# Performance work log

Hardware: AMD Instinct MI355X
Metric: run time of the kernel (lower is better)

The kernel has to match this reference:

```python
import jax, jax.numpy as jnp
import numpy as np

K = 7          # kernel_size
PAD = K // 2
NAZ, NEL = 12, 5
HID = 64
IC = 2         # input_channels == num_instruments
OC = 2         # output_channels (stereo)
EPS = 1e-5


def conv1d_same(x, w, b):
    # x: (N, Cin, T), w: (Cout, Cin, K) -> (N, Cout, T); cross-correlation like torch
    y = jax.lax.conv_general_dilated(x, w, (1,), 'SAME',
                                     dimension_numbers=('NCH', 'OIH', 'NCH'))
    return y + b[None, :, None]


def batchnorm(x, g, bt):
    # training-mode BatchNorm1d: biased batch stats over (N, T)
    mean = x.mean(axis=(0, 2), keepdims=True)
    var = x.var(axis=(0, 2), keepdims=True)
    return (x - mean) * jax.lax.rsqrt(var + EPS) * g[None, :, None] + bt[None, :, None]


def lrelu(x):
    return jnp.where(x >= 0, x, 0.2 * x)


def setup_inputs() -> dict:
    key = jax.random.key(0)
    ks = jax.random.split(key, 16)
    d = {}
    d['x'] = jax.random.normal(ks[0], (8, IC, 131072), dtype=jnp.float32)
    # spatial_param_net
    d['W1'] = jax.random.normal(ks[1], (HID, IC, K), dtype=jnp.float32) * 0.1
    d['b1'] = jnp.zeros((HID,), jnp.float32)
    d['g1'] = jnp.ones((HID,), jnp.float32)
    d['be1'] = jnp.zeros((HID,), jnp.float32)
    d['W2'] = jax.random.normal(ks[2], (2 * HID, HID, K), dtype=jnp.float32) * 0.05
    d['b2'] = jnp.zeros((2 * HID,), jnp.float32)
    d['g2'] = jnp.ones((2 * HID,), jnp.float32)
    d['be2'] = jnp.zeros((2 * HID,), jnp.float32)
    d['W3'] = jax.random.normal(ks[3], (IC * 3, 2 * HID, K), dtype=jnp.float32) * 0.05
    d['b3'] = jnp.zeros((IC * 3,), jnp.float32)
    # HRTF table: (num_azimuth*num_elevation, output_channels, K)
    d['hrtf'] = jax.random.normal(ks[4], (NAZ * NEL, OC, K), dtype=jnp.float32)
    # binaural_renderer (first conv in-channels = input_channels = 2)
    d['RW1'] = jax.random.normal(ks[5], (HID, IC, K), dtype=jnp.float32) * 0.1
    d['rb1'] = jnp.zeros((HID,), jnp.float32)
    d['rg1'] = jnp.ones((HID,), jnp.float32)
    d['rbe1'] = jnp.zeros((HID,), jnp.float32)
    d['RW2'] = jax.random.normal(ks[6], (2 * HID, HID, K), dtype=jnp.float32) * 0.05
    d['rb2'] = jnp.zeros((2 * HID,), jnp.float32)
    d['rg2'] = jnp.ones((2 * HID,), jnp.float32)
    d['rbe2'] = jnp.zeros((2 * HID,), jnp.float32)
    d['RW3'] = jax.random.normal(ks[7], (OC, 2 * HID, K), dtype=jnp.float32) * 0.05
    d['rb3'] = jnp.zeros((OC,), jnp.float32)
    return d


def reference(x, W1, b1, g1, be1, W2, b2, g2, be2, W3, b3, hrtf,
              RW1, rb1, rg1, rbe1, RW2, rb2, rg2, rbe2, RW3, rb3):
    B, I, T = x.shape
    # spatial parameter network
    h = lrelu(batchnorm(conv1d_same(x, W1, b1), g1, be1))
    h = lrelu(batchnorm(conv1d_same(h, W2, b2), g2, be2))
    sp = jnp.tanh(conv1d_same(h, W3, b3)).reshape(B, I, 3, T)
    # only t=0 of azimuth/elevation/distance is used (matches torch loop)
    az = (sp[:, :, 0, 0] + 1.0) * 0.5 * (NAZ - 1)
    el = (sp[:, :, 1, 0] + 1.0) * 0.5 * (NEL - 1)
    dist = (sp[:, :, 2, 0] + 1.0) * 0.5 * 0.9 + 0.1      # (B, I)
    az_i = jnp.clip(az.astype(jnp.int32), 0, NAZ - 1)
    el_i = jnp.clip(el.astype(jnp.int32), 0, NEL - 1)
    idx = el_i * NAZ + az_i                               # (B, I)
    wg = hrtf[idx]                                        # (B, I, OC, K) gathered filters
    # per-(b,i) conv1d with its gathered HRTF filter, scale by distance, sum over instruments
    xp = jnp.pad(x, ((0, 0), (0, 0), (PAD, PAD)))
    windows = jnp.stack([xp[:, :, k:k + T] for k in range(K)], axis=2)  # (B, I, K, T)
    summed = jnp.einsum('bikt,bick,bi->bct', windows, wg, dist)          # (B, OC, T)
    # binaural renderer
    h = lrelu(batchnorm(conv1d_same(summed, RW1, rb1), rg1, rbe1))
    h = lrelu(batchnorm(conv1d_same(h, RW2, rb2), rg2, rbe2))
    return jnp.tanh(conv1d_same(h, RW3, rb3))
```

## Files before the change

### kernel.cpp

```cpp
#include <hip/hip_runtime.h>
#include <hip/hip_fp16.h>
#include <cstddef>


#define TLEN 131072
#define NB 8
#define NICH 2
#define NHID 64
#define NH2 128
#define EPSV 1e-5f
#define CNTF 1048576.0f
#define FT 120
#define FGRID 1093
#define XCH 2048

typedef _Float16 f16x8 __attribute__((ext_vector_type(8)));
typedef float f32x4 __attribute__((ext_vector_type(4)));

__device__ __forceinline__ float lrelu(float v) { return fmaxf(v, 0.2f * v); }
__device__ __forceinline__ unsigned short h16(float v) {
  return __half_as_ushort(__float2half(v));
}
__device__ __forceinline__ float fh16(unsigned short u) {
  return __half2float(__ushort_as_half(u));
}
__device__ __forceinline__ float ftanh(float x) {
  float e = __expf(2.f * x);
  return 1.f - 2.f / (e + 1.f);
}

__global__ __launch_bounds__(256) void prep_weights(
    const float* __restrict__ W2c, const float* __restrict__ RW2c,
    const float* __restrict__ RW3c,
    const float* __restrict__ W1c, const float* __restrict__ RW1c,
    unsigned short* __restrict__ w2sp, unsigned short* __restrict__ w2re,
    unsigned short* __restrict__ w3g,
    unsigned short* __restrict__ w1sp, unsigned short* __restrict__ w1re)
{
  int e = blockIdx.x * 256 + threadIdx.x;
  if (e < 114688) {
    int e2 = (e >= 57344) ? e - 57344 : e;
    int frag = e2 >> 9, within = e2 & 511;
    int c = frag >> 3, mt = frag & 7;
    int mn = within >> 5, kk = within & 31;
    int o = mt * 16 + mn;
    int tap = c >> 1, ch = (c & 1) * 32 + kk;
    const float* src = (e >= 57344) ? RW2c : W2c;
    unsigned short* dst = (e >= 57344) ? w2re : w2sp;
    dst[e2] = h16(src[(o * 64 + ch) * 7 + tap]);
  } else if (e < 116736) {
    int e2 = e - 114688;
    int c = e2 >> 9, within = e2 & 511;
    int m = within >> 5, kk = within & 31;
    int ch = c * 32 + kk;
    w3g[e2] = (m < 14) ? h16(RW3c[((m / 7) * 128 + ch) * 7 + (m % 7)])
                       : (unsigned short)0;
  } else if (e < 120832) {
    int e2 = e - 116736;
    int which = (e2 >= 2048);
    int e3 = e2 & 2047;
    int m = e3 >> 9, w = e3 & 511;
    int mn = w >> 5, K = w & 31;
    int i = K >> 4, kk = K & 15;
    const float* src = which ? RW1c : W1c;
    unsigned short* dst = which ? w1re : w1sp;
    dst[e3] = (kk < 7) ? h16(src[(m * 16 + mn) * 14 + i * 7 + kk])
                       : (unsigned short)0;
  }
}

__global__ __launch_bounds__(256) void xcorr_stats(
    const float* __restrict__ z, float* __restrict__ partials)
{
  const int b = blockIdx.x >> 6;
  const int t0 = (blockIdx.x & 63) * XCH;
  __shared__ float zs[2][XCH + 8];
  __shared__ float redx[4][30];
  for (int i = 0; i < 2; ++i)
    for (int j = threadIdx.x; j < XCH + 7; j += 256) {
      int tg = t0 + j;
      zs[i][j] = (tg < TLEN) ? z[(b * 2 + i) * TLEN + tg] : 0.f;
    }
  __syncthreads();

  float acc[30];
  #pragma unroll
  for (int q = 0; q < 30; ++q) acc[q] = 0.f;
  const int tb = threadIdx.x * 8;
  #pragma unroll
  for (int tt = 0; tt < 8; ++tt) {
    int j = tb + tt;
    float z0 = zs[0][j], z1 = zs[1][j];
    acc[28] += z0; acc[29] += z1;
    #pragma unroll
    for (int d = 0; d < 7; ++d) {
      float a0 = zs[0][j + d], a1 = zs[1][j + d];
      acc[d]      += z0 * a0;
      acc[7 + d]  += z0 * a1;
      acc[14 + d] += z1 * a0;
      acc[21 + d] += z1 * a1;
    }
  }
  #pragma unroll
  for (int q = 0; q < 30; ++q)
    #pragma unroll
    for (int m = 1; m <= 32; m <<= 1)
      acc[q] += __shfl_xor(acc[q], m, 64);
  const int lane = threadIdx.x & 63, wv = threadIdx.x >> 6;
  if (lane == 0)
    #pragma unroll
    for (int q = 0; q < 30; ++q) redx[wv][q] = acc[q];
  __syncthreads();
  if (threadIdx.x < 30)
    partials[blockIdx.x * 30 + threadIdx.x] =
        redx[0][threadIdx.x] + redx[1][threadIdx.x] +
        redx[2][threadIdx.x] + redx[3][threadIdx.x];
}

__global__ __launch_bounds__(256) void assemble_coef1(
    const float* __restrict__ partials, int nblocks,
    const float* __restrict__ W1c, const float* __restrict__ b1c,
    const float* __restrict__ g, const float* __restrict__ be,
    float* __restrict__ coef)
{
  __shared__ float R[30];
  __shared__ float pr[8][30];
  __shared__ float w1s[64 * 14];
  for (int e = threadIdx.x; e < 64 * 14; e += 256) w1s[e] = W1c[e];
  if (threadIdx.x < 240) {
    int q = threadIdx.x % 30, chunk = threadIdx.x / 30;
    float s = 0.f;
    for (int j = chunk; j < nblocks; j += 8) s += partials[j * 30 + q];
    pr[chunk][q] = s;
  }
  __syncthreads();
  if (threadIdx.x < 30) {
    float s = 0.f;
    #pragma unroll
    for (int c = 0; c < 8; ++c) s += pr[c][threadIdx.x];
    R[threadIdx.x] = s;
  }
  __syncthreads();
  if (threadIdx.x < 64) {
    int o = threadIdx.x;
    const float* w = &w1s[o * 14];
    float b1v = b1c[o];
    float sy = 0.f;
    #pragma unroll
    for (int i = 0; i < 2; ++i)
      #pragma unroll
      for (int k = 0; k < 7; ++k) sy += w[i * 7 + k] * R[28 + i];
    float syy = 0.f;
    #pragma unroll
    for (int i = 0; i < 2; ++i)
      #pragma unroll
      for (int k = 0; k < 7; ++k) {
        float wv = w[i * 7 + k];
        #pragma unroll
        for (int i2 = 0; i2 < 2; ++i2)
          #pragma unroll
          for (int k2 = 0; k2 < 7; ++k2) {
            int d = k2 - k;
            float r = (d >= 0) ? R[i * 14 + i2 * 7 + d]
                               : R[i2 * 14 + i * 7 - d];
            syy += wv * w[i2 * 7 + k2] * r;
          }
      }
    float S1 = CNTF * b1v + sy;
    float S2 = 2.f * b1v * S1 - CNTF * b1v * b1v + syy;
    float mean = S1 / CNTF;
    float var = S2 / CNTF - mean * mean;
    float a = g[o] * rsqrtf(var + EPSV);
    coef[o] = a;
    coef[64 + o] = be[o] - mean * a;
  }
}

__global__ __launch_bounds__(256) void reduce_coef(
    const float* __restrict__ partials, int nblocks, int C,
    const float* __restrict__ bso,
    const float* __restrict__ g, const float* __restrict__ be,
    float* __restrict__ coef)
{
  const int c = blockIdx.x;
  float s = 0.f, ss = 0.f;
  for (int j = threadIdx.x; j < nblocks; j += 256) {
    s  += partials[j * 2 * C + c];
    ss += partials[j * 2 * C + C + c];
  }
  #pragma unroll
  for (int off = 32; off >= 1; off >>= 1) {
    s  += __shfl_down(s, off, 64);
    ss += __shfl_down(ss, off, 64);
  }
  __shared__ float rs[4], rss[4];
  const int lane = threadIdx.x & 63, wv = threadIdx.x >> 6;
  if (lane == 0) { rs[wv] = s; rss[wv] = ss; }
  __syncthreads();
  if (threadIdx.x == 0) {
    float st  = rs[0] + rs[1] + rs[2] + rs[3];
    float sst = rss[0] + rss[1] + rss[2] + rss[3];
    float mean = st / CNTF;
    float var  = sst / CNTF - mean * mean;
    float a = g[c] * rsqrtf(var + EPSV);
    float d = be[c] - mean * a;
    coef[c] = a;
    coef[C + c] = d;
    coef[2 * C + c] = d + a * bso[c];
  }
}

__device__ __forceinline__ void stage_x(
    int t0, int xoff, const float* __restrict__ xin, int b, float* xs)
{
  for (int e = threadIdx.x; e < 2 * 168; e += 256) {
    int i = e / 168, j = e % 168;
    int tg = t0 - xoff + j;
    xs[e] = (tg >= 0 && tg < TLEN) ? xin[(b * NICH + i) * TLEN + tg] : 0.f;
  }
}

template<int HOF>
__device__ __forceinline__ void h1_mfma(
    int t0, const float* xs, unsigned short* xw,
    const unsigned short* __restrict__ w1f,
    const float* __restrict__ coef1, const float* __restrict__ b1c,
    unsigned short* h1f)
{
  for (int e = threadIdx.x; e < 144 * 2; e += 256) {
    int n = e >> 1, i = e & 1;
    const float* xp = &xs[i * 168 + n];
    unsigned short hv[7];
    #pragma unroll
    for (int kk = 0; kk < 7; ++kk) hv[kk] = h16(xp[kk]);
    *(uint4*)(xw + n * 32 + i * 16) = make_uint4(
        hv[0] | ((unsigned)hv[1] << 16), hv[2] | ((unsigned)hv[3] << 16),
        hv[4] | ((unsigned)hv[5] << 16), (unsigned)hv[6]);
    *(uint4*)(xw + n * 32 + i * 16 + 8) = make_uint4(0, 0, 0, 0);
  }
  __syncthreads();

  const int lane = threadIdx.x & 63;
  const int wv = threadIdx.x >> 6;
  const int mn = lane & 15, quad = lane >> 4;
  f16x8 A1 = *(const f16x8*)(w1f + wv * 512 + mn * 32 + quad * 8);
  f32x4 acc1[9];
  #pragma unroll
  for (int nt = 0; nt < 9; ++nt) {
    f32x4 z = {0.f, 0.f, 0.f, 0.f};
    acc1[nt] = z;
  }
  #pragma unroll
  for (int nt = 0; nt < 9; ++nt) {
    f16x8 bb = *(const f16x8*)(xw + (nt * 16 + mn) * 32 + quad * 8);
    acc1[nt] = __builtin_amdgcn_mfma_f32_16x16x32_f16(A1, bb, acc1[nt], 0, 0, 0);
  }
  const int ch0 = wv * 16 + quad * 4;
  float a1v[4], dd[4];
  #pragma unroll
  for (int r = 0; r < 4; ++r) {
    a1v[r] = coef1[ch0 + r];
    dd[r]  = coef1[64 + ch0 + r] + a1v[r] * b1c[ch0 + r];
  }
  #pragma unroll
  for (int nt = 0; nt < 9; ++nt) {
    int n = nt * 16 + mn;
    int t = t0 - HOF + n;
    bool ok = (t >= 0) && (t < TLEN);
    unsigned us[4];
    #pragma unroll
    for (int r = 0; r < 4; ++r) {
      float v = lrelu(a1v[r] * acc1[nt][r] + dd[r]);
      us[r] = h16(ok ? v : 0.f);
    }
    *(uint2*)(h1f + n * 72 + ch0) =
        make_uint2(us[0] | (us[1] << 16), us[2] | (us[3] << 16));
  }
}

__global__ __launch_bounds__(256, 4) void conv2_stats_mfma(
    const float* __restrict__ xin,
    const unsigned short* __restrict__ w1f, const float* __restrict__ b1c,
    const float* __restrict__ coef1,
    const unsigned short* __restrict__ w2f,
    const float* __restrict__ b2c,
    float* __restrict__ partials)
{
  const int b  = blockIdx.x >> 10;
  const int t0 = (blockIdx.x & 1023) * 128;

  __shared__ __align__(16) char smem[31296];
  unsigned short* h1f = (unsigned short*)smem;
  float* xs = (float*)(smem + 20736);
  unsigned short* xw = (unsigned short*)(smem + 22080);
  float* redS = (float*)smem;
  float* redSS= (float*)(smem + 8704);

  stage_x(t0, 6, xin, b, xs);
  __syncthreads();
  h1_mfma<3>(t0, xs, xw, w1f, coef1, b1c, h1f);
  __syncthreads();

  const int lane = threadIdx.x & 63;
  const int wv = threadIdx.x >> 6;
  const int mn = lane & 15, quad = lane >> 4;

  f32x4 acc[2][8];
  #pragma unroll
  for (int mt = 0; mt < 2; ++mt)
    #pragma unroll
    for (int nt = 0; nt < 8; ++nt) {
      f32x4 z = {0.f, 0.f, 0.f, 0.f};
      acc[mt][nt] = z;
    }

  f16x8 ca[2], na[2];
  auto loadA = [&](int c, f16x8 (&A)[2]) {
    #pragma unroll
    for (int mt = 0; mt < 2; ++mt)
      A[mt] = *(const f16x8*)(w2f + (c * 8 + wv * 2 + mt) * 512 + mn * 32 + quad * 8);
  };
  loadA(0, ca);
  #pragma unroll
  for (int c = 0; c < 14; ++c) {
    if (c < 13) loadA(c + 1, na);
    const int tap = c >> 1;
    const int ch0 = (c & 1) * 32 + quad * 8;
    #pragma unroll
    for (int nt = 0; nt < 8; ++nt) {
      f16x8 bb = *(const f16x8*)(h1f + (nt * 16 + mn + tap) * 72 + ch0);
      acc[0][nt] = __builtin_amdgcn_mfma_f32_16x16x32_f16(ca[0], bb, acc[0][nt], 0, 0, 0);
      acc[1][nt] = __builtin_amdgcn_mfma_f32_16x16x32_f16(ca[1], bb, acc[1][nt], 0, 0, 0);
    }
    ca[0] = na[0]; ca[1] = na[1];
  }
  __syncthreads();

  #pragma unroll
  for (int mt = 0; mt < 2; ++mt)
    #pragma unroll
    for (int r = 0; r < 4; ++r) {
      int o = (wv * 2 + mt) * 16 + quad * 4 + r;
      float bo = b2c[o];
      float s = 0.f, ss = 0.f;
      #pragma unroll
      for (int nt = 0; nt < 8; ++nt) {
        float v = acc[mt][nt][r] + bo;
        s += v; ss += v * v;
      }
      redS[o * 17 + mn] = s;
      redSS[o * 17 + mn] = ss;
    }
  __syncthreads();
  {
    int o = threadIdx.x & 127;
    const float* src = (threadIdx.x < 128) ? redS : redSS;
    float s = 0.f;
    #pragma unroll
    for (int j = 0; j < 16; ++j) s += src[o * 17 + j];
    partials[blockIdx.x * 256 + threadIdx.x] = s;
  }
}

__global__ __launch_bounds__(256) void finalize_spatial(
    const float* __restrict__ x,
    const float* __restrict__ W1c, const float* __restrict__ b1c,
    const float* __restrict__ coef1,
    const float* __restrict__ W2c, const float* __restrict__ b2c,
    const float* __restrict__ coef2,
    const float* __restrict__ W3c, const float* __restrict__ b3c,
    const float* __restrict__ hrtf, float* __restrict__ wgbuf)
{
  __shared__ float xl[NB * 2 * 16];
  __shared__ float h1l[NB * 64 * 10];
  __shared__ float h2l[NB * NH2 * 4];
  __shared__ float sp[48];
  const int tid = threadIdx.x;
  {
    int bb = tid >> 5, i = (tid >> 4) & 1, j = tid & 15;
    int t = j - 6;
    xl[tid] = (t >= 0) ? x[(bb * 2 + i) * TLEN + t] : 0.f;
  }
  __syncthreads();
  for (int e = tid; e < NB * 64; e += 256) {
    int bb = e >> 6, ch = e & 63;
    float a1 = coef1[ch], d1 = coef1[64 + ch], bo = b1c[ch];
    for (int tt = 0; tt < 10; ++tt) {
      float acc = bo;
      #pragma unroll
      for (int i2 = 0; i2 < 2; ++i2)
        #pragma unroll
        for (int k = 0; k < 7; ++k)
          acc += xl[(bb * 2 + i2) * 16 + tt + k] * W1c[ch * 14 + i2 * 7 + k];
      float v = lrelu(a1 * acc + d1);
      h1l[(bb * 64 + ch) * 10 + tt] = (tt >= 3) ? v : 0.f;
    }
  }
  __syncthreads();
  for (int e = tid; e < NB * NH2; e += 256) {
    int bb = e >> 7, o = e & 127;
    float a2 = coef2[o], d2 = coef2[NH2 + o], bo = b2c[o];
    float acc[4] = {bo, bo, bo, bo};
    for (int i = 0; i < 64; ++i)
      #pragma unroll
      for (int k = 0; k < 7; ++k) {
        float w = W2c[(o * 64 + i) * 7 + k];
        #pragma unroll
        for (int t = 0; t < 4; ++t)
          acc[t] += h1l[(bb * 64 + i) * 10 + t + k] * w;
      }
    #pragma unroll
    for (int t = 0; t < 4; ++t)
      h2l[(bb * NH2 + o) * 4 + t] = lrelu(a2 * acc[t] + d2);
  }
  __syncthreads();
  if (tid < 48) {
    int bb = tid / 6, c3 = tid % 6;
    float acc = b3c[c3];
    for (int c = 0; c < NH2; ++c)
      #pragma unroll
      for (int k = 3; k < 7; ++k)
        acc += h2l[(bb * NH2 + c) * 4 + (k - 3)] * W3c[(c3 * NH2 + c) * 7 + k];
    sp[tid] = tanhf(acc);
  }
  __syncthreads();
  if (tid < 16) {
    int bb = tid >> 1, i = tid & 1;
    float az = (sp[bb * 6 + i * 3 + 0] + 1.f) * 0.5f * 11.f;
    float el = (sp[bb * 6 + i * 3 + 1] + 1.f) * 0.5f * 4.f;
    float dist = (sp[bb * 6 + i * 3 + 2] + 1.f) * 0.5f * 0.9f + 0.1f;
    int azi = min(max((int)az, 0), 11);
    int eli = min(max((int)el, 0), 4);
    int idx = eli * 12 + azi;
    for (int e = 0; e < 14; ++e)
      wgbuf[(bb * 2 + i) * 14 + e] = hrtf[idx * 14 + e] * dist;
  }
}

__global__ __launch_bounds__(256) void mix_kernel(
    const float* __restrict__ x, const float* __restrict__ wgbuf,
    float* __restrict__ summed)
{
  const int b = blockIdx.x >> 7;
  const int t0 = (blockIdx.x & 127) * 1024 + threadIdx.x * 4;
  float wv[2][2][7];
  #pragma unroll
  for (int i = 0; i < 2; ++i)
    #pragma unroll
    for (int c = 0; c < 2; ++c)
      #pragma unroll
      for (int k = 0; k < 7; ++k)
        wv[i][c][k] = wgbuf[(b * 2 + i) * 14 + c * 7 + k];
  float acc[2][4] = {{0.f, 0.f, 0.f, 0.f}, {0.f, 0.f, 0.f, 0.f}};
  #pragma unroll
  for (int i = 0; i < 2; ++i) {
    float xl[12];
    #pragma unroll
    for (int j = 0; j < 12; ++j) {
      int tg = t0 - 4 + j;
      xl[j] = (tg >= 0 && tg < TLEN) ? x[(b * 2 + i) * TLEN + tg] : 0.f;
    }
    #pragma unroll
    for (int c = 0; c < 2; ++c)
      #pragma unroll
      for (int k = 0; k < 7; ++k)
        #pragma unroll
        for (int tt = 0; tt < 4; ++tt)
          acc[c][tt] += xl[tt + k + 1] * wv[i][c][k];
  }
  #pragma unroll
  for (int c = 0; c < 2; ++c)
    *reinterpret_cast<float4*>(&summed[(b * 2 + c) * TLEN + t0]) =
        make_float4(acc[c][0], acc[c][1], acc[c][2], acc[c][3]);
}

__global__ __launch_bounds__(256, 4) void conv2_final_mfma(
    const float* __restrict__ xin,
    const unsigned short* __restrict__ w1f, const float* __restrict__ b1c,
    const float* __restrict__ coef1,
    const unsigned short* __restrict__ w2f,
    const float* __restrict__ coef2,
    const unsigned short* __restrict__ w3g, const float* __restrict__ rb3c,
    float* __restrict__ out)
{
  const int b  = blockIdx.y;
  const int t0 = blockIdx.x * FT;

  __shared__ __align__(16) char smem[39936];
  unsigned short* h1f = (unsigned short*)smem;
  float* xs = (float*)(smem + 20736);
  unsigned short* xw = (unsigned short*)(smem + 22080);
  unsigned short* h2t = (unsigned short*)smem;
  unsigned short* dq  = (unsigned short*)(smem + 34816);

  stage_x(t0, 9, xin, b, xs);
  __syncthreads();
  h1_mfma<6>(t0, xs, xw, w1f, coef1, b1c, h1f);
  __syncthreads();

  const int lane = threadIdx.x & 63;
  const int wv = threadIdx.x >> 6;
  const int mn = lane & 15, quad = lane >> 4;

  f32x4 acc[2][8];
  #pragma unroll
  for (int mt = 0; mt < 2; ++mt)
    #pragma unroll
    for (int nt = 0; nt < 8; ++nt) {
      f32x4 z = {0.f, 0.f, 0.f, 0.f};
      acc[mt][nt] = z;
    }

  f16x8 ca[2], na[2];
  auto loadA = [&](int c, f16x8 (&A)[2]) {
    #pragma unroll
    for (int mt = 0; mt < 2; ++mt)
      A[mt] = *(const f16x8*)(w2f + (c * 8 + wv * 2 + mt) * 512 + mn * 32 + quad * 8);
  };
  loadA(0, ca);
  #pragma unroll
  for (int c = 0; c < 14; ++c) {
    if (c < 13) loadA(c + 1, na);
    const int tap = c >> 1;
    const int ch0 = (c & 1) * 32 + quad * 8;
    #pragma unroll
    for (int nt = 0; nt < 8; ++nt) {
      f16x8 bb = *(const f16x8*)(h1f + (nt * 16 + mn + tap) * 72 + ch0);
      acc[0][nt] = __builtin_amdgcn_mfma_f32_16x16x32_f16(ca[0], bb, acc[0][nt], 0, 0, 0);
      acc[1][nt] = __builtin_amdgcn_mfma_f32_16x16x32_f16(ca[1], bb, acc[1][nt], 0, 0, 0);
    }
    ca[0] = na[0]; ca[1] = na[1];
  }

  float a2v[2][4], dd2[2][4];
  #pragma unroll
  for (int mt = 0; mt < 2; ++mt)
    #pragma unroll
    for (int r = 0; r < 4; ++r) {
      int o = (wv * 2 + mt) * 16 + quad * 4 + r;
      a2v[mt][r] = coef2[o];
      dd2[mt][r] = coef2[2 * NH2 + o];
    }
  __syncthreads();

  #pragma unroll
  for (int nt = 0; nt < 8; ++nt) {
    int jp = nt * 16 + mn;
    int t = t0 - 3 + jp;
    bool ok = (t >= 0) && (t < TLEN);
    #pragma unroll
    for (int mt = 0; mt < 2; ++mt) {
      int obase = (wv * 2 + mt) * 16 + quad * 4;
      unsigned us[4];
      #pragma unroll
      for (int r = 0; r < 4; ++r) {
        float v = lrelu(a2v[mt][r] * acc[mt][nt][r] + dd2[mt][r]);
        us[r] = h16(ok ? v : 0.f);
      }
      *(uint2*)(h2t + jp * 136 + obase) =
          make_uint2(us[0] | (us[1] << 16), us[2] | (us[3] << 16));
    }
  }
  __syncthreads();

  const int nt0 = wv * 2;
  f32x4 acc3[2];
  #pragma unroll
  for (int i = 0; i < 2; ++i) {
    f32x4 z = {0.f, 0.f, 0.f, 0.f};
    acc3[i] = z;
  }
  #pragma unroll
  for (int c = 0; c < 4; ++c) {
    f16x8 A3 = *(const f16x8*)(w3g + c * 512 + mn * 32 + quad * 8);
    #pragma unroll
    for (int i = 0; i < 2; ++i) {
      f16x8 bb = *(const f16x8*)(h2t + ((nt0 + i) * 16 + mn) * 136 + c * 32 + quad * 8);
      acc3[i] = __builtin_amdgcn_mfma_f32_16x16x32_f16(A3, bb, acc3[i], 0, 0, 0);
    }
  }
  #pragma unroll
  for (int i = 0; i < 2; ++i) {
    int n = (nt0 + i) * 16 + mn;
    unsigned us[4];
    #pragma unroll
    for (int r = 0; r < 4; ++r) us[r] = h16(acc3[i][r]);
    *(uint2*)(dq + n * 20 + quad * 4) =
        make_uint2(us[0] | (us[1] << 16), us[2] | (us[3] << 16));
  }
  __syncthreads();

  {
    int tid = threadIdx.x;
    if (tid < 240) {
      int oc = (tid >= FT) ? 1 : 0;
      int u = tid - oc * FT;
      float s = rb3c[oc];
      #pragma unroll
      for (int tap = 0; tap < 7; ++tap)
        s += fh16(dq[(u + tap) * 20 + oc * 7 + tap]);
      int t = t0 + u;
      if (t < TLEN) out[(b * 2 + oc) * TLEN + t] = ftanh(s);
    }
  }
}

extern "C" void kernel_launch(void* const* d_in, const int* in_sizes, int n_in,
                              void* d_out, int out_size, void* d_ws, size_t ws_size,
                              hipStream_t stream)
{
  (void)in_sizes; (void)n_in; (void)out_size; (void)ws_size;
  const float* x    = (const float*)d_in[0];
  const float* W1   = (const float*)d_in[1];
  const float* b1   = (const float*)d_in[2];
  const float* g1   = (const float*)d_in[3];
  const float* be1  = (const float*)d_in[4];
  const float* W2   = (const float*)d_in[5];
  const float* b2   = (const float*)d_in[6];
  const float* g2   = (const float*)d_in[7];
  const float* be2  = (const float*)d_in[8];
  const float* W3   = (const float*)d_in[9];
  const float* b3   = (const float*)d_in[10];
  const float* hrtf = (const float*)d_in[11];
  const float* RW1  = (const float*)d_in[12];
  const float* rb1  = (const float*)d_in[13];
  const float* rg1  = (const float*)d_in[14];
  const float* rbe1 = (const float*)d_in[15];
  const float* RW2  = (const float*)d_in[16];
  const float* rb2  = (const float*)d_in[17];
  const float* rg2  = (const float*)d_in[18];
  const float* rbe2 = (const float*)d_in[19];
  const float* RW3  = (const float*)d_in[20];
  const float* rb3  = (const float*)d_in[21];
  float* out = (float*)d_out;

  float* partialsB = (float*)d_out;

  char* ws = (char*)d_ws;
  float* partialsA      = (float*)(ws + 0);
  float* summed         = (float*)(ws + 524288);
  float* coef1          = (float*)(ws + 8912896);
  float* coef2          = (float*)(ws + 8913408);
  float* coefR1         = (float*)(ws + 8914944);
  float* coefR2         = (float*)(ws + 8915456);
  float* wgbuf          = (float*)(ws + 8916992);
  unsigned short* w2sp  = (unsigned short*)(ws + 8918016);
  unsigned short* w2re  = (unsigned short*)(ws + 9032704);
  unsigned short* w3g   = (unsigned short*)(ws + 9147392);
  unsigned short* w1sp  = (unsigned short*)(ws + 9151488);
  unsigned short* w1re  = (unsigned short*)(ws + 9155584);

  prep_weights<<<472, 256, 0, stream>>>(W2, RW2, RW3, W1, RW1,
                                        w2sp, w2re, w3g, w1sp, w1re);
  xcorr_stats<<<512, 256, 0, stream>>>(x, partialsA);
  assemble_coef1<<<1, 256, 0, stream>>>(partialsA, 512, W1, b1, g1, be1, coef1);
  conv2_stats_mfma<<<8192, 256, 0, stream>>>(x, w1sp, b1, coef1, w2sp, b2,
                                             partialsB);
  reduce_coef<<<128, 256, 0, stream>>>(partialsB, 8192, 128, b2, g2, be2, coef2);
  finalize_spatial<<<1, 256, 0, stream>>>(x, W1, b1, coef1, W2, b2, coef2,
                                          W3, b3, hrtf, wgbuf);
  mix_kernel<<<1024, 256, 0, stream>>>(x, wgbuf, summed);
  xcorr_stats<<<512, 256, 0, stream>>>(summed, partialsA);
  assemble_coef1<<<1, 256, 0, stream>>>(partialsA, 512, RW1, rb1, rg1, rbe1, coefR1);
  conv2_stats_mfma<<<8192, 256, 0, stream>>>(summed, w1re, rb1, coefR1,
                                             w2re, rb2, partialsB);
  reduce_coef<<<128, 256, 0, stream>>>(partialsB, 8192, 128, rb2, rg2, rbe2, coefR2);
  conv2_final_mfma<<<dim3(FGRID, NB), 256, 0, stream>>>(
      summed, w1re, rb1, coefR1, w2re, coefR2, w3g, rb3, out);
}
```

Baseline: 648.9 us.

## Store renderer conv2 activations in fp16 and skip recomputation in final pass

The renderer's stats pass now also writes the pre-norm conv2 output (fp16, 128 channels per sample) to a large workspace buffer. The final pass then only applies the BN affine and leaky ReLU, runs conv3 and writes the output, instead of recomputing conv1 and conv2. This swaps a large MFMA recompute for about 256MB of extra global write and read traffic. It falls back to the old path when the workspace is too small.

```diff
diff --git a/kernel.cpp b/kernel.cpp
--- a/kernel.cpp
+++ b/kernel.cpp
@@ -278,21 +278,24 @@
   }
 }
 
+template<bool SAVE>
 __global__ __launch_bounds__(256, 4) void conv2_stats_mfma(
     const float* __restrict__ xin,
     const unsigned short* __restrict__ w1f, const float* __restrict__ b1c,
     const float* __restrict__ coef1,
     const unsigned short* __restrict__ w2f,
     const float* __restrict__ b2c,
-    float* __restrict__ partials)
+    float* __restrict__ partials,
+    unsigned short* __restrict__ h2out)
 {
   const int b  = blockIdx.x >> 10;
   const int t0 = (blockIdx.x & 1023) * 128;
 
-  __shared__ __align__(16) char smem[31296];
+  __shared__ __align__(16) char smem[34816];
   unsigned short* h1f = (unsigned short*)smem;
   float* xs = (float*)(smem + 20736);
   unsigned short* xw = (unsigned short*)(smem + 22080);
+  unsigned short* h2t = (unsigned short*)smem;
   float* redS = (float*)smem;
   float* redSS= (float*)(smem + 8704);
 
@@ -335,6 +338,29 @@
     ca[0] = na[0]; ca[1] = na[1];
   }
   __syncthreads();
+
+  if (SAVE) {
+    #pragma unroll
+    for (int nt = 0; nt < 8; ++nt) {
+      int jp = nt * 16 + mn;
+      #pragma unroll
+      for (int mt = 0; mt < 2; ++mt) {
+        int obase = (wv * 2 + mt) * 16 + quad * 4;
+        unsigned us[4];
+        #pragma unroll
+        for (int r = 0; r < 4; ++r) us[r] = h16(acc[mt][nt][r]);
+        *(uint2*)(h2t + jp * 136 + obase) =
+            make_uint2(us[0] | (us[1] << 16), us[2] | (us[3] << 16));
+      }
+    }
+    __syncthreads();
+    for (int e = threadIdx.x; e < 2048; e += 256) {
+      int row = e >> 4, c8 = (e & 15) * 8;
+      *(uint4*)(h2out + (size_t)(b * TLEN + t0 + row) * 128 + c8) =
+          *(const uint4*)(h2t + row * 136 + c8);
+    }
+    __syncthreads();
+  }
 
   #pragma unroll
   for (int mt = 0; mt < 2; ++mt)
@@ -605,11 +631,99 @@
   }
 }
 
+__global__ __launch_bounds__(256, 4) void render_final_light(
+    const unsigned short* __restrict__ h2s,
+    const float* __restrict__ coef2,
+    const unsigned short* __restrict__ w3g, const float* __restrict__ rb3c,
+    float* __restrict__ out)
+{
+  const int b  = blockIdx.y;
+  const int t0 = blockIdx.x * FT;
+
+  __shared__ __align__(16) char smem[39936];
+  unsigned short* h2t = (unsigned short*)smem;
+  unsigned short* dq  = (unsigned short*)(smem + 34816);
+
+  const int c8 = (threadIdx.x & 15) * 8;
+  float a2r[8], d2r[8];
+  #pragma unroll
+  for (int j = 0; j < 8; ++j) {
+    a2r[j] = coef2[c8 + j];
+    d2r[j] = coef2[2 * NH2 + c8 + j];
+  }
+  for (int e = threadIdx.x; e < 2048; e += 256) {
+    int row = e >> 4;
+    int t = t0 - 3 + row;
+    uint4 pk = make_uint4(0, 0, 0, 0);
+    if (t >= 0 && t < TLEN) {
+      uint4 rv = *(const uint4*)(h2s + ((size_t)(b * TLEN + t) * 128 + c8));
+      unsigned w[4] = {rv.x, rv.y, rv.z, rv.w};
+      unsigned ow[4];
+      #pragma unroll
+      for (int j = 0; j < 4; ++j) {
+        float vlo = lrelu(a2r[2 * j] * fh16((unsigned short)(w[j] & 0xffff)) +
+                          d2r[2 * j]);
+        float vhi = lrelu(a2r[2 * j + 1] * fh16((unsigned short)(w[j] >> 16)) +
+                          d2r[2 * j + 1]);
+        ow[j] = (unsigned)h16(vlo) | ((unsigned)h16(vhi) << 16);
+      }
+      pk = make_uint4(ow[0], ow[1], ow[2], ow[3]);
+    }
+    *(uint4*)(h2t + row * 136 + c8) = pk;
+  }
+  __syncthreads();
+
+  const int lane = threadIdx.x & 63;
+  const int wv = threadIdx.x >> 6;
+  const int mn = lane & 15, quad = lane >> 4;
+
+  const int nt0 = wv * 2;
+  f32x4 acc3[2];
+  #pragma unroll
+  for (int i = 0; i < 2; ++i) {
+    f32x4 z = {0.f, 0.f, 0.f, 0.f};
+    acc3[i] = z;
+  }
+  #pragma unroll
+  for (int c = 0; c < 4; ++c) {
+    f16x8 A3 = *(const f16x8*)(w3g + c * 512 + mn * 32 + quad * 8);
+    #pragma unroll
+    for (int i = 0; i < 2; ++i) {
+      f16x8 bb = *(const f16x8*)(h2t + ((nt0 + i) * 16 + mn) * 136 + c * 32 + quad * 8);
+      acc3[i] = __builtin_amdgcn_mfma_f32_16x16x32_f16(A3, bb, acc3[i], 0, 0, 0);
+    }
+  }
+  #pragma unroll
+  for (int i = 0; i < 2; ++i) {
+    int n = (nt0 + i) * 16 + mn;
+    unsigned us[4];
+    #pragma unroll
+    for (int r = 0; r < 4; ++r) us[r] = h16(acc3[i][r]);
+    *(uint2*)(dq + n * 20 + quad * 4) =
+        make_uint2(us[0] | (us[1] << 16), us[2] | (us[3] << 16));
+  }
+  __syncthreads();
+
+  {
+    int tid = threadIdx.x;
+    if (tid < 240) {
+      int oc = (tid >= FT) ? 1 : 0;
+      int u = tid - oc * FT;
+      float s = rb3c[oc];
+      #pragma unroll
+      for (int tap = 0; tap < 7; ++tap)
+        s += fh16(dq[(u + tap) * 20 + oc * 7 + tap]);
+      int t = t0 + u;
+      if (t < TLEN) out[(b * 2 + oc) * TLEN + t] = ftanh(s);
+    }
+  }
+}
+
 extern "C" void kernel_launch(void* const* d_in, const int* in_sizes, int n_in,
                               void* d_out, int out_size, void* d_ws, size_t ws_size,
                               hipStream_t stream)
 {
-  (void)in_sizes; (void)n_in; (void)out_size; (void)ws_size;
+  (void)in_sizes; (void)n_in; (void)out_size;
   const float* x    = (const float*)d_in[0];
   const float* W1   = (const float*)d_in[1];
   const float* b1   = (const float*)d_in[2];
@@ -649,22 +763,35 @@
   unsigned short* w3g   = (unsigned short*)(ws + 9147392);
   unsigned short* w1sp  = (unsigned short*)(ws + 9151488);
   unsigned short* w1re  = (unsigned short*)(ws + 9155584);
+  unsigned short* h2s   = (unsigned short*)(ws + 16777216);
+  const size_t WS_NEEDED_BIG = 16777216ull + 268435456ull;
+  const bool big = ws_size >= WS_NEEDED_BIG;
 
   prep_weights<<<472, 256, 0, stream>>>(W2, RW2, RW3, W1, RW1,
                                         w2sp, w2re, w3g, w1sp, w1re);
   xcorr_stats<<<512, 256, 0, stream>>>(x, partialsA);
   assemble_coef1<<<1, 256, 0, stream>>>(partialsA, 512, W1, b1, g1, be1, coef1);
-  conv2_stats_mfma<<<8192, 256, 0, stream>>>(x, w1sp, b1, coef1, w2sp, b2,
-                                             partialsB);
+  conv2_stats_mfma<false><<<8192, 256, 0, stream>>>(x, w1sp, b1, coef1, w2sp,
+                                                    b2, partialsB, nullptr);
   reduce_coef<<<128, 256, 0, stream>>>(partialsB, 8192, 128, b2, g2, be2, coef2);
   finalize_spatial<<<1, 256, 0, stream>>>(x, W1, b1, coef1, W2, b2, coef2,
                                           W3, b3, hrtf, wgbuf);
   mix_kernel<<<1024, 256, 0, stream>>>(x, wgbuf, summed);
   xcorr_stats<<<512, 256, 0, stream>>>(summed, partialsA);
   assemble_coef1<<<1, 256, 0, stream>>>(partialsA, 512, RW1, rb1, rg1, rbe1, coefR1);
-  conv2_stats_mfma<<<8192, 256, 0, stream>>>(summed, w1re, rb1, coefR1,
-                                             w2re, rb2, partialsB);
+  if (big) {
+    conv2_stats_mfma<true><<<8192, 256, 0, stream>>>(summed, w1re, rb1, coefR1,
+                                                     w2re, rb2, partialsB, h2s);
+  } else {
+    conv2_stats_mfma<false><<<8192, 256, 0, stream>>>(summed, w1re, rb1, coefR1,
+                                                      w2re, rb2, partialsB, nullptr);
+  }
   reduce_coef<<<128, 256, 0, stream>>>(partialsB, 8192, 128, rb2, rg2, rbe2, coefR2);
-  conv2_final_mfma<<<dim3(FGRID, NB), 256, 0, stream>>>(
-      summed, w1re, rb1, coefR1, w2re, coefR2, w3g, rb3, out);
-}
+  if (big) {
+    render_final_light<<<dim3(FGRID, NB), 256, 0, stream>>>(
+        h2s, coefR2, w3g, rb3, out);
+  } else {
+    conv2_final_mfma<<<dim3(FGRID, NB), 256, 0, stream>>>(
+        summed, w1re, rb1, coefR1, w2re, coefR2, w3g, rb3, out);
+  }
+}
```

Result: no change. 660.6 us (+1.8%).

## Cache renderer layer-1 activations in workspace and reuse them in final pass

Applied to the files above, without the earlier changes.

The renderer's stats pass now writes its fp16 first-layer activations (B×T×64) to a large workspace buffer. A new final kernel loads those activations instead of recomputing conv1 from the summed signal. This removes the repeated layer-1 MFMA work at the cost of roughly 256 MB of extra global memory traffic (one write, one read). The path only runs when the workspace is large enough, and otherwise falls back to the old kernel.

```diff
diff --git a/kernel.cpp b/kernel.cpp
--- a/kernel.cpp
+++ b/kernel.cpp
@@ -278,13 +278,15 @@
   }
 }
 
+template<int SAVE>
 __global__ __launch_bounds__(256, 4) void conv2_stats_mfma(
     const float* __restrict__ xin,
     const unsigned short* __restrict__ w1f, const float* __restrict__ b1c,
     const float* __restrict__ coef1,
     const unsigned short* __restrict__ w2f,
     const float* __restrict__ b2c,
-    float* __restrict__ partials)
+    float* __restrict__ partials,
+    unsigned short* __restrict__ h1out)
 {
   const int b  = blockIdx.x >> 10;
   const int t0 = (blockIdx.x & 1023) * 128;
@@ -333,6 +335,14 @@
       acc[1][nt] = __builtin_amdgcn_mfma_f32_16x16x32_f16(ca[1], bb, acc[1][nt], 0, 0, 0);
     }
     ca[0] = na[0]; ca[1] = na[1];
+  }
+
+  if (SAVE == 1) {
+    for (int e = threadIdx.x; e < 1024; e += 256) {
+      int row = e >> 3, c8 = (e & 7) * 8;
+      *(uint4*)(h1out + ((size_t)(b * TLEN + t0 + row) * 64 + c8)) =
+          *(const uint4*)(h1f + (row + 3) * 72 + c8);
+    }
   }
   __syncthreads();
 
@@ -474,6 +484,125 @@
         make_float4(acc[c][0], acc[c][1], acc[c][2], acc[c][3]);
 }
 
+__device__ __forceinline__ void final_tail(
+    int b, int t0, f32x4 (&acc)[2][8],
+    const float* __restrict__ coef2,
+    const unsigned short* __restrict__ w3g, const float* __restrict__ rb3c,
+    unsigned short* h2t, unsigned short* dq, float* __restrict__ out)
+{
+  const int lane = threadIdx.x & 63;
+  const int wv = threadIdx.x >> 6;
+  const int mn = lane & 15, quad = lane >> 4;
+
+  float a2v[2][4], dd2[2][4];
+  #pragma unroll
+  for (int mt = 0; mt < 2; ++mt)
+    #pragma unroll
+    for (int r = 0; r < 4; ++r) {
+      int o = (wv * 2 + mt) * 16 + quad * 4 + r;
+      a2v[mt][r] = coef2[o];
+      dd2[mt][r] = coef2[2 * NH2 + o];
+    }
+  __syncthreads();
+
+  #pragma unroll
+  for (int nt = 0; nt < 8; ++nt) {
+    int jp = nt * 16 + mn;
+    int t = t0 - 3 + jp;
+    bool ok = (t >= 0) && (t < TLEN);
+    #pragma unroll
+    for (int mt = 0; mt < 2; ++mt) {
+      int obase = (wv * 2 + mt) * 16 + quad * 4;
+      unsigned us[4];
+      #pragma unroll
+      for (int r = 0; r < 4; ++r) {
+        float v = lrelu(a2v[mt][r] * acc[mt][nt][r] + dd2[mt][r]);
+        us[r] = h16(ok ? v : 0.f);
+      }
+      *(uint2*)(h2t + jp * 136 + obase) =
+          make_uint2(us[0] | (us[1] << 16), us[2] | (us[3] << 16));
+    }
+  }
+  __syncthreads();
+
+  const int nt0 = wv * 2;
+  f32x4 acc3[2];
+  #pragma unroll
+  for (int i = 0; i < 2; ++i) {
+    f32x4 z = {0.f, 0.f, 0.f, 0.f};
+    acc3[i] = z;
+  }
+  #pragma unroll
+  for (int c = 0; c < 4; ++c) {
+    f16x8 A3 = *(const f16x8*)(w3g + c * 512 + mn * 32 + quad * 8);
+    #pragma unroll
+    for (int i = 0; i < 2; ++i) {
+      f16x8 bb = *(const f16x8*)(h2t + ((nt0 + i) * 16 + mn) * 136 + c * 32 + quad * 8);
+      acc3[i] = __builtin_amdgcn_mfma_f32_16x16x32_f16(A3, bb, acc3[i], 0, 0, 0);
+    }
+  }
+  #pragma unroll
+  for (int i = 0; i < 2; ++i) {
+    int n = (nt0 + i) * 16 + mn;
+    unsigned us[4];
+    #pragma unroll
+    for (int r = 0; r < 4; ++r) us[r] = h16(acc3[i][r]);
+    *(uint2*)(dq + n * 20 + quad * 4) =
+        make_uint2(us[0] | (us[1] << 16), us[2] | (us[3] << 16));
+  }
+  __syncthreads();
+
+  {
+    int tid = threadIdx.x;
+    if (tid < 240) {
+      int oc = (tid >= FT) ? 1 : 0;
+      int u = tid - oc * FT;
+      float s = rb3c[oc];
+      #pragma unroll
+      for (int tap = 0; tap < 7; ++tap)
+        s += fh16(dq[(u + tap) * 20 + oc * 7 + tap]);
+      int t = t0 + u;
+      if (t < TLEN) out[(b * 2 + oc) * TLEN + t] = ftanh(s);
+    }
+  }
+}
+
+__device__ __forceinline__ void conv2_loop(
+    const unsigned short* h1f, const unsigned short* __restrict__ w2f,
+    f32x4 (&acc)[2][8])
+{
+  const int lane = threadIdx.x & 63;
+  const int wv = threadIdx.x >> 6;
+  const int mn = lane & 15, quad = lane >> 4;
+  #pragma unroll
+  for (int mt = 0; mt < 2; ++mt)
+    #pragma unroll
+    for (int nt = 0; nt < 8; ++nt) {
+      f32x4 z = {0.f, 0.f, 0.f, 0.f};
+      acc[mt][nt] = z;
+    }
+  f16x8 ca[2], na[2];
+  auto loadA = [&](int c, f16x8 (&A)[2]) {
+    #pragma unroll
+    for (int mt = 0; mt < 2; ++mt)
+      A[mt] = *(const f16x8*)(w2f + (c * 8 + wv * 2 + mt) * 512 + mn * 32 + quad * 8);
+  };
+  loadA(0, ca);
+  #pragma unroll
+  for (int c = 0; c < 14; ++c) {
+    if (c < 13) loadA(c + 1, na);
+    const int tap = c >> 1;
+    const int ch0 = (c & 1) * 32 + quad * 8;
+    #pragma unroll
+    for (int nt = 0; nt < 8; ++nt) {
+      f16x8 bb = *(const f16x8*)(h1f + (nt * 16 + mn + tap) * 72 + ch0);
+      acc[0][nt] = __builtin_amdgcn_mfma_f32_16x16x32_f16(ca[0], bb, acc[0][nt], 0, 0, 0);
+      acc[1][nt] = __builtin_amdgcn_mfma_f32_16x16x32_f16(ca[1], bb, acc[1][nt], 0, 0, 0);
+    }
+    ca[0] = na[0]; ca[1] = na[1];
+  }
+}
+
 __global__ __launch_bounds__(256, 4) void conv2_final_mfma(
     const float* __restrict__ xin,
     const unsigned short* __restrict__ w1f, const float* __restrict__ b1c,
@@ -498,118 +627,46 @@
   h1_mfma<6>(t0, xs, xw, w1f, coef1, b1c, h1f);
   __syncthreads();
 
-  const int lane = threadIdx.x & 63;
-  const int wv = threadIdx.x >> 6;
-  const int mn = lane & 15, quad = lane >> 4;
-
   f32x4 acc[2][8];
-  #pragma unroll
-  for (int mt = 0; mt < 2; ++mt)
-    #pragma unroll
-    for (int nt = 0; nt < 8; ++nt) {
-      f32x4 z = {0.f, 0.f, 0.f, 0.f};
-      acc[mt][nt] = z;
-    }
-
-  f16x8 ca[2], na[2];
-  auto loadA = [&](int c, f16x8 (&A)[2]) {
-    #pragma unroll
-    for (int mt = 0; mt < 2; ++mt)
-      A[mt] = *(const f16x8*)(w2f + (c * 8 + wv * 2 + mt) * 512 + mn * 32 + quad * 8);
-  };
-  loadA(0, ca);
-  #pragma unroll
-  for (int c = 0; c < 14; ++c) {
-    if (c < 13) loadA(c + 1, na);
-    const int tap = c >> 1;
-    const int ch0 = (c & 1) * 32 + quad * 8;
-    #pragma unroll
-    for (int nt = 0; nt < 8; ++nt) {
-      f16x8 bb = *(const f16x8*)(h1f + (nt * 16 + mn + tap) * 72 + ch0);
-      acc[0][nt] = __builtin_amdgcn_mfma_f32_16x16x32_f16(ca[0], bb, acc[0][nt], 0, 0, 0);
-      acc[1][nt] = __builtin_amdgcn_mfma_f32_16x16x32_f16(ca[1], bb, acc[1][nt], 0, 0, 0);
-    }
-    ca[0] = na[0]; ca[1] = na[1];
-  }
-
-  float a2v[2][4], dd2[2][4];
-  #pragma unroll
-  for (int mt = 0; mt < 2; ++mt)
-    #pragma unroll
-    for (int r = 0; r < 4; ++r) {
-      int o = (wv * 2 + mt) * 16 + quad * 4 + r;
-      a2v[mt][r] = coef2[o];
-      dd2[mt][r] = coef2[2 * NH2 + o];
-    }
-  __syncthreads();
-
-  #pragma unroll
-  for (int nt = 0; nt < 8; ++nt) {
-    int jp = nt * 16 + mn;
-    int t = t0 - 3 + jp;
-    bool ok = (t >= 0) && (t < TLEN);
-    #pragma unroll
-    for (int mt = 0; mt < 2; ++mt) {
-      int obase = (wv * 2 + mt) * 16 + quad * 4;
-      unsigned us[4];
-      #pragma unroll
-      for (int r = 0; r < 4; ++r) {
-        float v = lrelu(a2v[mt][r] * acc[mt][nt][r] + dd2[mt][r]);
-        us[r] = h16(ok ? v : 0.f);
-      }
-      *(uint2*)(h2t + jp * 136 + obase) =
-          make_uint2(us[0] | (us[1] << 16), us[2] | (us[3] << 16));
-    }
-  }
-  __syncthreads();
-
-  const int nt0 = wv * 2;
-  f32x4 acc3[2];
-  #pragma unroll
-  for (int i = 0; i < 2; ++i) {
-    f32x4 z = {0.f, 0.f, 0.f, 0.f};
-    acc3[i] = z;
-  }
-  #pragma unroll
-  for (int c = 0; c < 4; ++c) {
-    f16x8 A3 = *(const f16x8*)(w3g + c * 512 + mn * 32 + quad * 8);
-    #pragma unroll
-    for (int i = 0; i < 2; ++i) {
-      f16x8 bb = *(const f16x8*)(h2t + ((nt0 + i) * 16 + mn) * 136 + c * 32 + quad * 8);
-      acc3[i] = __builtin_amdgcn_mfma_f32_16x16x32_f16(A3, bb, acc3[i], 0, 0, 0);
-    }
-  }
-  #pragma unroll
-  for (int i = 0; i < 2; ++i) {
-    int n = (nt0 + i) * 16 + mn;
-    unsigned us[4];
-    #pragma unroll
-    for (int r = 0; r < 4; ++r) us[r] = h16(acc3[i][r]);
-    *(uint2*)(dq + n * 20 + quad * 4) =
-        make_uint2(us[0] | (us[1] << 16), us[2] | (us[3] << 16));
-  }
-  __syncthreads();
-
-  {
-    int tid = threadIdx.x;
-    if (tid < 240) {
-      int oc = (tid >= FT) ? 1 : 0;
-      int u = tid - oc * FT;
-      float s = rb3c[oc];
-      #pragma unroll
-      for (int tap = 0; tap < 7; ++tap)
-        s += fh16(dq[(u + tap) * 20 + oc * 7 + tap]);
-      int t = t0 + u;
-      if (t < TLEN) out[(b * 2 + oc) * TLEN + t] = ftanh(s);
-    }
-  }
+  conv2_loop(h1f, w2f, acc);
+  final_tail(b, t0, acc, coef2, w3g, rb3c, h2t, dq, out);
+}
+
+__global__ __launch_bounds__(256, 4) void conv2_final_h1(
+    const unsigned short* __restrict__ h1g,
+    const unsigned short* __restrict__ w2f,
+    const float* __restrict__ coef2,
+    const unsigned short* __restrict__ w3g, const float* __restrict__ rb3c,
+    float* __restrict__ out)
+{
+  const int b  = blockIdx.y;
+  const int t0 = blockIdx.x * FT;
+
+  __shared__ __align__(16) char smem[39936];
+  unsigned short* h1f = (unsigned short*)smem;
+  unsigned short* h2t = (unsigned short*)smem;
+  unsigned short* dq  = (unsigned short*)(smem + 34816);
+
+  for (int e = threadIdx.x; e < 144 * 8; e += 256) {
+    int r = e >> 3, c8 = (e & 7) * 8;
+    int t = t0 - 6 + r;
+    uint4 v = make_uint4(0, 0, 0, 0);
+    if (t >= 0 && t < TLEN)
+      v = *(const uint4*)(h1g + ((size_t)(b * TLEN + t) * 64 + c8));
+    *(uint4*)(h1f + r * 72 + c8) = v;
+  }
+  __syncthreads();
+
+  f32x4 acc[2][8];
+  conv2_loop(h1f, w2f, acc);
+  final_tail(b, t0, acc, coef2, w3g, rb3c, h2t, dq, out);
 }
 
 extern "C" void kernel_launch(void* const* d_in, const int* in_sizes, int n_in,
                               void* d_out, int out_size, void* d_ws, size_t ws_size,
                               hipStream_t stream)
 {
-  (void)in_sizes; (void)n_in; (void)out_size; (void)ws_size;
+  (void)in_sizes; (void)n_in; (void)out_size;
   const float* x    = (const float*)d_in[0];
   const float* W1   = (const float*)d_in[1];
   const float* b1   = (const float*)d_in[2];
@@ -649,22 +706,35 @@
   unsigned short* w3g   = (unsigned short*)(ws + 9147392);
   unsigned short* w1sp  = (unsigned short*)(ws + 9151488);
   unsigned short* w1re  = (unsigned short*)(ws + 9155584);
+  unsigned short* h1g   = (unsigned short*)(ws + 16777216);
+  const size_t WS_NEEDED_MID = 16777216ull + 134217728ull;
+  const bool mid = ws_size >= WS_NEEDED_MID;
 
   prep_weights<<<472, 256, 0, stream>>>(W2, RW2, RW3, W1, RW1,
                                         w2sp, w2re, w3g, w1sp, w1re);
   xcorr_stats<<<512, 256, 0, stream>>>(x, partialsA);
   assemble_coef1<<<1, 256, 0, stream>>>(partialsA, 512, W1, b1, g1, be1, coef1);
-  conv2_stats_mfma<<<8192, 256, 0, stream>>>(x, w1sp, b1, coef1, w2sp, b2,
-                                             partialsB);
+  conv2_stats_mfma<0><<<8192, 256, 0, stream>>>(x, w1sp, b1, coef1, w2sp,
+                                                b2, partialsB, nullptr);
   reduce_coef<<<128, 256, 0, stream>>>(partialsB, 8192, 128, b2, g2, be2, coef2);
   finalize_spatial<<<1, 256, 0, stream>>>(x, W1, b1, coef1, W2, b2, coef2,
                                           W3, b3, hrtf, wgbuf);
   mix_kernel<<<1024, 256, 0, stream>>>(x, wgbuf, summed);
   xcorr_stats<<<512, 256, 0, stream>>>(summed, partialsA);
   assemble_coef1<<<1, 256, 0, stream>>>(partialsA, 512, RW1, rb1, rg1, rbe1, coefR1);
-  conv2_stats_mfma<<<8192, 256, 0, stream>>>(summed, w1re, rb1, coefR1,
-                                             w2re, rb2, partialsB);
+  if (mid) {
+    conv2_stats_mfma<1><<<8192, 256, 0, stream>>>(summed, w1re, rb1, coefR1,
+                                                  w2re, rb2, partialsB, h1g);
+  } else {
+    conv2_stats_mfma<0><<<8192, 256, 0, stream>>>(summed, w1re, rb1, coefR1,
+                                                  w2re, rb2, partialsB, nullptr);
+  }
   reduce_coef<<<128, 256, 0, stream>>>(partialsB, 8192, 128, rb2, rg2, rbe2, coefR2);
-  conv2_final_mfma<<<dim3(FGRID, NB), 256, 0, stream>>>(
-      summed, w1re, rb1, coefR1, w2re, coefR2, w3g, rb3, out);
-}
+  if (mid) {
+    conv2_final_h1<<<dim3(FGRID, NB), 256, 0, stream>>>(
+        h1g, w2re, coefR2, w3g, rb3, out);
+  } else {
+    conv2_final_mfma<<<dim3(FGRID, NB), 256, 0, stream>>>(
+        summed, w1re, rb1, coefR1, w2re, coefR2, w3g, rb3, out);
+  }
+}
```

Result: no change. 655.4 us (+1.0%).
